# Optimization experiments

Hardware: AMD Instinct MI355X
Metric: run time of the kernel (lower is better)

## Reference

```python
import jax, jax.numpy as jnp
import numpy as np

N, E, DIN, DOUT = 50000, 800000, 64, 64


def setup_inputs() -> dict:
    key = jax.random.key(0)
    k1, k2, k3, k4, k5 = jax.random.split(key, 5)
    x = jax.random.normal(k1, (N, DIN), dtype=jnp.float32)
    edge_index = jax.random.randint(k2, (2, E), 0, N, dtype=jnp.int64)
    edge_attr = jax.random.uniform(k3, (E,), dtype=jnp.float32)
    # PyG GCNConv params: linear weight (no bias in lin) + conv bias
    W = jax.random.normal(k4, (DIN, DOUT), dtype=jnp.float32) / np.sqrt(DIN)
    b = jax.random.normal(k5, (DOUT,), dtype=jnp.float32) * 0.01
    return {
        "x": x,
        "edge_index": edge_index,
        "edge_attr": edge_attr,
        "return_attention_weights": 0,
        "W": W,
        "b": b,
    }


def reference(x, edge_index, edge_attr, return_attention_weights, W, b):
    # GCNConv(add_self_loops=False, normalize=True), edge_weight = ones.
    # edge_attr / return_attention_weights are unused by the original module.
    n = x.shape[0]
    src, dst = edge_index[0], edge_index[1]
    # in-degree on destination nodes (gcn_norm with ones edge weights)
    deg = jax.ops.segment_sum(jnp.ones_like(src, dtype=x.dtype), dst, num_segments=n)
    dis = jnp.where(deg > 0, jax.lax.rsqrt(jnp.maximum(deg, 1)), jnp.zeros_like(deg))
    norm = dis[src] * dis[dst]  # [E]
    h = x @ W  # [N, DOUT] -- transform before aggregation (in < out would flip, equal here)
    msg = h[src] * norm[:, None]  # [E, DOUT]
    out = jax.ops.segment_sum(msg, dst, num_segments=n) + b  # [N, DOUT]
    return out
```

## Files before the change

### kernel.cpp

```cpp
#include <hip/hip_runtime.h>
#include <stdint.h>


#define CAP   64
#define BSH   7
#define NBMAX 512
#define EPB   4096
#define BCAP  2816
#define NGEMM 1024

typedef float vf4 __attribute__((ext_vector_type(4)));

__device__ __forceinline__ int probe_is64(const void* eidx, int n_edges, int n_nodes) {
    int lane = threadIdx.x & 63;
    const long long* p = (const long long*)eidx;
    int cnt = n_edges < 64 ? n_edges : 64;
    long long v = p[lane % cnt];
    bool ok = (v >= 0) && (v < (long long)n_nodes);
    return (__ballot(ok) == ~0ull) ? 1 : 0;
}

__device__ __forceinline__ int load_idx(const void* eidx, long long i, int is64) {
    if (is64) return (int)((const long long*)eidx)[i];
    return ((const int*)eidx)[i];
}

__device__ __forceinline__ unsigned short f2bf(float v) {
    unsigned u = __float_as_uint(v);
    unsigned r = (u + 0x7fffu + ((u >> 16) & 1u)) >> 16;
    return (unsigned short)r;
}

__device__ __forceinline__ float bflo(unsigned u) { return __uint_as_float(u << 16); }
__device__ __forceinline__ float bfhi(unsigned u) { return __uint_as_float(u & 0xffff0000u); }

__global__ __launch_bounds__(256) void k_front(
    const float* __restrict__ x, const float* __restrict__ W,
    unsigned* __restrict__ h32w,
    const void* eidx, unsigned* __restrict__ tails,
    unsigned* __restrict__ buckets,
    int n, int ne, int nb, int nchunks, int binb)
{
    const int tid = (int)threadIdx.x;
    const int bid = (int)blockIdx.x;

    if (bid < binb) {
        __shared__ unsigned histo[NBMAX];
        __shared__ unsigned base[NBMAX];
        int is64 = probe_is64(eidx, ne, n);
        for (int c = bid; c < nchunks; c += binb) {
            __syncthreads();
            for (int i = tid; i < NBMAX; i += 256) histo[i] = 0u;
            __syncthreads();
            unsigned pk[16], rk[16];
            long long e0 = (long long)c * EPB + tid;
            #pragma unroll
            for (int j = 0; j < 16; ++j) {
                long long e = e0 + 256 * j;
                if (e < (long long)ne) {
                    int s = load_idx(eidx, e, is64);
                    int t = load_idx(eidx, (long long)ne + e, is64);
                    pk[j] = ((unsigned)t << 16) | (unsigned)s;
                    rk[j] = atomicAdd(&histo[(unsigned)t >> BSH], 1u);
                } else { pk[j] = 0u; rk[j] = 0xFFFFFFFFu; }
            }
            __syncthreads();
            unsigned U = tails[NBMAX];
            for (int b2 = tid; b2 < nb; b2 += 256) {
                unsigned cc = histo[b2];
                base[b2] = cc ? (atomicAdd(&tails[b2], cc) - U) : 0u;
            }
            __syncthreads();
            #pragma unroll
            for (int j = 0; j < 16; ++j) {
                if (rk[j] != 0xFFFFFFFFu) {
                    unsigned bk = pk[j] >> (16 + BSH);
                    unsigned slot = base[bk] + rk[j];
                    if (slot < (unsigned)BCAP)
                        buckets[(size_t)bk * BCAP + slot] = pk[j];
                }
            }
        }
        return;
    }

    __shared__ float Ws[64][66];
    __shared__ float xs[16][64];
    for (int j = 0; j < 4; ++j) {
        int q = tid + 256 * j;
        int r = q >> 4, c4 = (q & 15) * 4;
        float4 w4 = ((const float4*)W)[q];
        Ws[r][c4] = w4.x; Ws[r][c4 + 1] = w4.y; Ws[r][c4 + 2] = w4.z; Ws[r][c4 + 3] = w4.w;
    }
    const int ntile = (n + 15) >> 4;
    const int f2 = (tid & 31) * 2;
    const int rg = tid >> 5;
    for (int tile = bid - binb; tile < ntile; tile += NGEMM) {
        __syncthreads();
        int row0 = tile << 4;
        {
            int r = tid >> 4, c4 = (tid & 15) * 4;
            int row = row0 + r;
            float4 v4 = (row < n) ? ((const float4*)x)[(size_t)row * 16 + (tid & 15)]
                                  : make_float4(0.f, 0.f, 0.f, 0.f);
            xs[r][c4] = v4.x; xs[r][c4 + 1] = v4.y; xs[r][c4 + 2] = v4.z; xs[r][c4 + 3] = v4.w;
        }
        __syncthreads();
        float a00 = 0.f, a01 = 0.f, a10 = 0.f, a11 = 0.f;
        for (int k = 0; k < 64; ++k) {
            float w0 = Ws[k][f2], w1 = Ws[k][f2 + 1];
            float xa = xs[rg][k], xb = xs[rg + 8][k];
            a00 += xa * w0; a01 += xa * w1;
            a10 += xb * w0; a11 += xb * w1;
        }
        int rowA = row0 + rg, rowB = rowA + 8;
        if (rowA < n)
            h32w[(size_t)rowA * 32 + (f2 >> 1)] =
                (unsigned)f2bf(a00) | ((unsigned)f2bf(a01) << 16);
        if (rowB < n)
            h32w[(size_t)rowB * 32 + (f2 >> 1)] =
                (unsigned)f2bf(a10) | ((unsigned)f2bf(a11) << 16);
    }
}

__global__ __launch_bounds__(256) void k_place2(
    const unsigned* __restrict__ tails,
    const unsigned* __restrict__ buckets,
    unsigned short* __restrict__ csr16,
    float* __restrict__ dis, unsigned char* __restrict__ endc, int n)
{
    __shared__ unsigned degL[1 << BSH];
    const int tid = (int)threadIdx.x;
    const int b = (int)blockIdx.x;
    const int t0 = b << BSH;
    if (tid < (1 << BSH)) degL[tid] = 0u;
    __syncthreads();
    unsigned U = tails[NBMAX];
    unsigned cnt = tails[b] - U;
    if (cnt > (unsigned)BCAP) cnt = (unsigned)BCAP;
    for (unsigned i = (unsigned)tid; i < cnt; i += 256) {
        unsigned p = buckets[(size_t)b * BCAP + i];
        unsigned dl = (p >> 16) & ((1u << BSH) - 1);
        unsigned r = atomicAdd(&degL[dl], 1u);
        if (r < (unsigned)CAP)
            csr16[((size_t)(t0 + (int)dl)) * CAP + r] = (unsigned short)(p & 0xFFFFu);
    }
    __syncthreads();
    if (tid < (1 << BSH)) {
        int node = t0 + tid;
        if (node < n) {
            unsigned d = degL[tid];
            dis[node] = d ? rsqrtf((float)d) : 0.f;
            endc[node] = (unsigned char)(d < (unsigned)CAP ? d : (unsigned)CAP);
        }
    }
}

__global__ __launch_bounds__(256) void k_place_direct(
    const void* eidx, unsigned* __restrict__ deg,
    unsigned short* __restrict__ csr16, int n, int ne)
{
    int is64 = probe_is64(eidx, ne, n);
    unsigned base = deg[n];
    int e = (int)blockIdx.x * 256 + (int)threadIdx.x;
    if (e >= ne) return;
    int s = load_idx(eidx, e, is64);
    int t = load_idx(eidx, (long long)ne + e, is64);
    unsigned r = atomicAdd(&deg[t], 1u) - base;
    if (r < (unsigned)CAP)
        csr16[(size_t)t * CAP + r] = (unsigned short)s;
}

__global__ __launch_bounds__(256) void k_finalize_direct(
    const unsigned* __restrict__ deg,
    float* __restrict__ dis, unsigned char* __restrict__ endc, int n)
{
    int i = (int)blockIdx.x * 256 + (int)threadIdx.x;
    if (i >= n) return;
    unsigned base = deg[n];
    unsigned cnt = deg[i] - base;
    dis[i] = cnt ? rsqrtf((float)cnt) : 0.f;
    endc[i] = (unsigned char)(cnt < (unsigned)CAP ? cnt : (unsigned)CAP);
}

__global__ __launch_bounds__(256) void k_aggregate(
    const float* __restrict__ dis,
    const unsigned char* __restrict__ endc,
    const unsigned short* __restrict__ csr16,
    const uint2* __restrict__ h64,
    const float* __restrict__ bias,
    float* __restrict__ out, int n)
{
    int wid  = (int)threadIdx.x >> 6;
    int lane = (int)threadIdx.x & 63;
    int t = (int)blockIdx.x * 4 + wid;
    if (t >= n) return;
    int allsrc = (int)csr16[(size_t)t * CAP + lane];
    unsigned end = endc[t];
    float dis_t = dis[t];
    int f = lane & 15, q = lane >> 4;
    float a0 = 0.f, a1 = 0.f, a2 = 0.f, a3 = 0.f;

    unsigned K4 = end >> 4;
    for (unsigned k = 0; k < K4; ++k) {
        int j = q + (int)(k << 4);
        int s0 = __shfl(allsrc, j, 64);
        int s1 = __shfl(allsrc, j + 4, 64);
        int s2 = __shfl(allsrc, j + 8, 64);
        int s3 = __shfl(allsrc, j + 12, 64);
        float w0 = dis[s0], w1 = dis[s1], w2 = dis[s2], w3 = dis[s3];
        uint2 u0 = h64[(size_t)s0 * 16 + f];
        uint2 u1 = h64[(size_t)s1 * 16 + f];
        uint2 u2 = h64[(size_t)s2 * 16 + f];
        uint2 u3 = h64[(size_t)s3 * 16 + f];
        a0 += w0 * bflo(u0.x) + w1 * bflo(u1.x) + w2 * bflo(u2.x) + w3 * bflo(u3.x);
        a1 += w0 * bfhi(u0.x) + w1 * bfhi(u1.x) + w2 * bfhi(u2.x) + w3 * bfhi(u3.x);
        a2 += w0 * bflo(u0.y) + w1 * bflo(u1.y) + w2 * bflo(u2.y) + w3 * bflo(u3.y);
        a3 += w0 * bfhi(u0.y) + w1 * bfhi(u1.y) + w2 * bfhi(u2.y) + w3 * bfhi(u3.y);
    }
    unsigned rem = end & 15u;
    if (rem) {
        unsigned jb = K4 << 4;
        for (unsigned k = 0; k < 4; ++k) {
            unsigned jj = jb + (k << 2) + (unsigned)q;
            bool valid = jj < end;
            int s = __shfl(allsrc, (int)(jj & 63u), 64);
            s = valid ? s : 0;
            float w = valid ? dis[s] : 0.f;
            uint2 u = h64[(size_t)s * 16 + f];
            a0 += w * bflo(u.x);
            a1 += w * bfhi(u.x);
            a2 += w * bflo(u.y);
            a3 += w * bfhi(u.y);
        }
    }
    a0 += __shfl_xor(a0, 16, 64); a0 += __shfl_xor(a0, 32, 64);
    a1 += __shfl_xor(a1, 16, 64); a1 += __shfl_xor(a1, 32, 64);
    a2 += __shfl_xor(a2, 16, 64); a2 += __shfl_xor(a2, 32, 64);
    a3 += __shfl_xor(a3, 16, 64); a3 += __shfl_xor(a3, 32, 64);
    if (q == 0) {
        float4 bb = ((const float4*)bias)[f];
        float4 o;
        o.x = a0 * dis_t + bb.x;
        o.y = a1 * dis_t + bb.y;
        o.z = a2 * dis_t + bb.z;
        o.w = a3 * dis_t + bb.w;
        ((float4*)out)[(size_t)t * 16 + f] = o;
    }
}

extern "C" void kernel_launch(void* const* d_in, const int* in_sizes, int n_in,
                              void* d_out, int out_size, void* d_ws, size_t ws_size,
                              hipStream_t stream) {
    const float* x   = (const float*)d_in[0];
    const void* eidx = d_in[1];
    const float* W   = (const float*)d_in[4];
    const float* b   = (const float*)d_in[5];
    float* out       = (float*)d_out;

    const int n  = in_sizes[0] / 64;
    const int ne = in_sizes[2];
    const int nb = (n + (1 << BSH) - 1) >> BSH;
    const int nchunks = (ne + EPB - 1) / EPB;
    const int binb = nchunks;

    auto al = [](size_t v) { return (v + 255) & ~(size_t)255; };

    size_t need = al((size_t)(NBMAX + 1) * 4) + al((size_t)nb * BCAP * 4)
                + al((size_t)n * CAP * 2) + al((size_t)n * 32 * 4)
                + al((size_t)n * 4) + al((size_t)n);
    bool binned = (ws_size >= need) && (nb <= NBMAX);

    char* base = (char*)d_ws;
    size_t off = 0;
    unsigned*       tails   = (unsigned*)(base + off);       off = al(off + (size_t)(NBMAX + 1) * 4);
    unsigned*       buckets = (unsigned*)(base + off);       off = al(off + (size_t)nb * BCAP * 4);
    unsigned short* csr16   = (unsigned short*)(base + off); off = al(off + (size_t)n * CAP * 2);
    unsigned*       h32     = (unsigned*)(base + off);       off = al(off + (size_t)n * 32 * 4);
    float*          dis     = (float*)(base + off);          off = al(off + (size_t)n * 4);
    unsigned char*  endc    = (unsigned char*)(base + off);  off = al(off + (size_t)n);

    if (binned) {
        k_front<<<binb + NGEMM, 256, 0, stream>>>(x, W, h32, eidx, tails, buckets,
                                                  n, ne, nb, nchunks, binb);
        k_place2<<<nb, 256, 0, stream>>>(tails, buckets, csr16, dis, endc, n);
    } else {
        unsigned* deg = buckets;
        k_front<<<0 + NGEMM, 256, 0, stream>>>(x, W, h32, eidx, tails, buckets,
                                               n, ne, nb, 0, 0);
        k_place_direct<<<(ne + 255) / 256, 256, 0, stream>>>(eidx, deg, csr16, n, ne);
        k_finalize_direct<<<(n + 255) / 256, 256, 0, stream>>>(deg, dis, endc, n);
    }
    k_aggregate<<<(n + 3) / 4, 256, 0, stream>>>(dis, endc, csr16, (const uint2*)h32, b, out, n);
}
```

Baseline: 136.0 us.

## Split fused bin+GEMM kernel and use 4x4 register-tiled GEMM

The combined front kernel, which ran edge binning and the x@W transform in different blocks of one launch, is split into two separate kernels. The GEMM now processes 64 rows per block, with each thread computing a 4x4 output tile using vector loads of W from shared memory. This replaces the old 16-row tile with a 2x2 per-thread tile, so each shared-memory load feeds more FMAs. The split removes the overlap that came from co-scheduling binning and GEMM blocks and adds one extra kernel launch.

```diff
diff --git a/kernel.cpp b/kernel.cpp
--- a/kernel.cpp
+++ b/kernel.cpp
@@ -7,7 +7,6 @@
 #define NBMAX 512
 #define EPB   4096
 #define BCAP  2816
-#define NGEMM 1024
 
 typedef float vf4 __attribute__((ext_vector_type(4)));
 
@@ -34,92 +33,102 @@
 __device__ __forceinline__ float bflo(unsigned u) { return __uint_as_float(u << 16); }
 __device__ __forceinline__ float bfhi(unsigned u) { return __uint_as_float(u & 0xffff0000u); }
 
-__global__ __launch_bounds__(256) void k_front(
+__global__ __launch_bounds__(256) void k_bin(
+    const void* eidx, unsigned* __restrict__ tails,
+    unsigned* __restrict__ buckets, int n, int ne, int nb)
+{
+    __shared__ unsigned histo[NBMAX];
+    __shared__ unsigned base[NBMAX];
+    const int tid = (int)threadIdx.x;
+    for (int i = tid; i < NBMAX; i += 256) histo[i] = 0u;
+    int is64 = probe_is64(eidx, ne, n);
+    __syncthreads();
+
+    unsigned pk[16], rk[16];
+    long long e0 = (long long)blockIdx.x * EPB + tid;
+    #pragma unroll
+    for (int j = 0; j < 16; ++j) {
+        long long e = e0 + 256 * j;
+        if (e < (long long)ne) {
+            int s = load_idx(eidx, e, is64);
+            int t = load_idx(eidx, (long long)ne + e, is64);
+            pk[j] = ((unsigned)t << 16) | (unsigned)s;
+            rk[j] = atomicAdd(&histo[(unsigned)t >> BSH], 1u);
+        } else { pk[j] = 0u; rk[j] = 0xFFFFFFFFu; }
+    }
+    __syncthreads();
+    unsigned U = tails[NBMAX];
+    for (int b2 = tid; b2 < nb; b2 += 256) {
+        unsigned cc = histo[b2];
+        base[b2] = cc ? (atomicAdd(&tails[b2], cc) - U) : 0u;
+    }
+    __syncthreads();
+    #pragma unroll
+    for (int j = 0; j < 16; ++j) {
+        if (rk[j] != 0xFFFFFFFFu) {
+            unsigned bk = pk[j] >> (16 + BSH);
+            unsigned slot = base[bk] + rk[j];
+            if (slot < (unsigned)BCAP)
+                buckets[(size_t)bk * BCAP + slot] = pk[j];
+        }
+    }
+}
+
+__global__ __launch_bounds__(256) void k_gemm(
     const float* __restrict__ x, const float* __restrict__ W,
-    unsigned* __restrict__ h32w,
-    const void* eidx, unsigned* __restrict__ tails,
-    unsigned* __restrict__ buckets,
-    int n, int ne, int nb, int nchunks, int binb)
-{
+    unsigned* __restrict__ h32w, int n)
+{
+    __shared__ float Ws[64 * 64];
+    __shared__ float xs[64 * 68];
     const int tid = (int)threadIdx.x;
-    const int bid = (int)blockIdx.x;
-
-    if (bid < binb) {
-        __shared__ unsigned histo[NBMAX];
-        __shared__ unsigned base[NBMAX];
-        int is64 = probe_is64(eidx, ne, n);
-        for (int c = bid; c < nchunks; c += binb) {
-            __syncthreads();
-            for (int i = tid; i < NBMAX; i += 256) histo[i] = 0u;
-            __syncthreads();
-            unsigned pk[16], rk[16];
-            long long e0 = (long long)c * EPB + tid;
-            #pragma unroll
-            for (int j = 0; j < 16; ++j) {
-                long long e = e0 + 256 * j;
-                if (e < (long long)ne) {
-                    int s = load_idx(eidx, e, is64);
-                    int t = load_idx(eidx, (long long)ne + e, is64);
-                    pk[j] = ((unsigned)t << 16) | (unsigned)s;
-                    rk[j] = atomicAdd(&histo[(unsigned)t >> BSH], 1u);
-                } else { pk[j] = 0u; rk[j] = 0xFFFFFFFFu; }
-            }
-            __syncthreads();
-            unsigned U = tails[NBMAX];
-            for (int b2 = tid; b2 < nb; b2 += 256) {
-                unsigned cc = histo[b2];
-                base[b2] = cc ? (atomicAdd(&tails[b2], cc) - U) : 0u;
-            }
-            __syncthreads();
-            #pragma unroll
-            for (int j = 0; j < 16; ++j) {
-                if (rk[j] != 0xFFFFFFFFu) {
-                    unsigned bk = pk[j] >> (16 + BSH);
-                    unsigned slot = base[bk] + rk[j];
-                    if (slot < (unsigned)BCAP)
-                        buckets[(size_t)bk * BCAP + slot] = pk[j];
-                }
-            }
-        }
-        return;
-    }
-
-    __shared__ float Ws[64][66];
-    __shared__ float xs[16][64];
+    const int row0 = (int)blockIdx.x * 64;
+
+    for (int j = 0; j < 4; ++j) {
+        int q = tid + 256 * j;
+        float4 w4 = ((const float4*)W)[q];
+        float* d = &Ws[q * 4];
+        d[0] = w4.x; d[1] = w4.y; d[2] = w4.z; d[3] = w4.w;
+    }
     for (int j = 0; j < 4; ++j) {
         int q = tid + 256 * j;
         int r = q >> 4, c4 = (q & 15) * 4;
-        float4 w4 = ((const float4*)W)[q];
-        Ws[r][c4] = w4.x; Ws[r][c4 + 1] = w4.y; Ws[r][c4 + 2] = w4.z; Ws[r][c4 + 3] = w4.w;
-    }
-    const int ntile = (n + 15) >> 4;
-    const int f2 = (tid & 31) * 2;
-    const int rg = tid >> 5;
-    for (int tile = bid - binb; tile < ntile; tile += NGEMM) {
-        __syncthreads();
-        int row0 = tile << 4;
-        {
-            int r = tid >> 4, c4 = (tid & 15) * 4;
-            int row = row0 + r;
-            float4 v4 = (row < n) ? ((const float4*)x)[(size_t)row * 16 + (tid & 15)]
-                                  : make_float4(0.f, 0.f, 0.f, 0.f);
-            xs[r][c4] = v4.x; xs[r][c4 + 1] = v4.y; xs[r][c4 + 2] = v4.z; xs[r][c4 + 3] = v4.w;
+        int row = row0 + r;
+        float4 v4 = (row < n) ? ((const float4*)x)[(size_t)row * 16 + (q & 15)]
+                              : make_float4(0.f, 0.f, 0.f, 0.f);
+        float* d = &xs[r * 68 + c4];
+        d[0] = v4.x; d[1] = v4.y; d[2] = v4.z; d[3] = v4.w;
+    }
+    __syncthreads();
+
+    const int fg = tid & 15, rg = tid >> 4;
+    const int r0 = rg * 4;
+    float acc[4][4];
+    #pragma unroll
+    for (int i = 0; i < 4; ++i)
+        #pragma unroll
+        for (int j = 0; j < 4; ++j) acc[i][j] = 0.f;
+
+    #pragma unroll 4
+    for (int k = 0; k < 64; ++k) {
+        vf4 w4 = *(const vf4*)&Ws[k * 64 + fg * 4];
+        float x0 = xs[(r0 + 0) * 68 + k];
+        float x1 = xs[(r0 + 1) * 68 + k];
+        float x2 = xs[(r0 + 2) * 68 + k];
+        float x3 = xs[(r0 + 3) * 68 + k];
+        acc[0][0] += x0 * w4.x; acc[0][1] += x0 * w4.y; acc[0][2] += x0 * w4.z; acc[0][3] += x0 * w4.w;
+        acc[1][0] += x1 * w4.x; acc[1][1] += x1 * w4.y; acc[1][2] += x1 * w4.z; acc[1][3] += x1 * w4.w;
+        acc[2][0] += x2 * w4.x; acc[2][1] += x2 * w4.y; acc[2][2] += x2 * w4.z; acc[2][3] += x2 * w4.w;
+        acc[3][0] += x3 * w4.x; acc[3][1] += x3 * w4.y; acc[3][2] += x3 * w4.z; acc[3][3] += x3 * w4.w;
+    }
+    #pragma unroll
+    for (int i = 0; i < 4; ++i) {
+        int row = row0 + r0 + i;
+        if (row < n) {
+            h32w[(size_t)row * 32 + fg * 2] =
+                (unsigned)f2bf(acc[i][0]) | ((unsigned)f2bf(acc[i][1]) << 16);
+            h32w[(size_t)row * 32 + fg * 2 + 1] =
+                (unsigned)f2bf(acc[i][2]) | ((unsigned)f2bf(acc[i][3]) << 16);
         }
-        __syncthreads();
-        float a00 = 0.f, a01 = 0.f, a10 = 0.f, a11 = 0.f;
-        for (int k = 0; k < 64; ++k) {
-            float w0 = Ws[k][f2], w1 = Ws[k][f2 + 1];
-            float xa = xs[rg][k], xb = xs[rg + 8][k];
-            a00 += xa * w0; a01 += xa * w1;
-            a10 += xb * w0; a11 += xb * w1;
-        }
-        int rowA = row0 + rg, rowB = rowA + 8;
-        if (rowA < n)
-            h32w[(size_t)rowA * 32 + (f2 >> 1)] =
-                (unsigned)f2bf(a00) | ((unsigned)f2bf(a01) << 16);
-        if (rowB < n)
-            h32w[(size_t)rowB * 32 + (f2 >> 1)] =
-                (unsigned)f2bf(a10) | ((unsigned)f2bf(a11) << 16);
     }
 }
 
@@ -262,7 +271,6 @@
     const int ne = in_sizes[2];
     const int nb = (n + (1 << BSH) - 1) >> BSH;
     const int nchunks = (ne + EPB - 1) / EPB;
-    const int binb = nchunks;
 
     auto al = [](size_t v) { return (v + 255) & ~(size_t)255; };
 
@@ -281,13 +289,12 @@
     unsigned char*  endc    = (unsigned char*)(base + off);  off = al(off + (size_t)n);
 
     if (binned) {
-        k_front<<<binb + NGEMM, 256, 0, stream>>>(x, W, h32, eidx, tails, buckets,
-                                                  n, ne, nb, nchunks, binb);
+        k_bin<<<nchunks, 256, 0, stream>>>(eidx, tails, buckets, n, ne, nb);
+        k_gemm<<<(n + 63) / 64, 256, 0, stream>>>(x, W, h32, n);
         k_place2<<<nb, 256, 0, stream>>>(tails, buckets, csr16, dis, endc, n);
     } else {
         unsigned* deg = buckets;
-        k_front<<<0 + NGEMM, 256, 0, stream>>>(x, W, h32, eidx, tails, buckets,
-                                               n, ne, nb, 0, 0);
+        k_gemm<<<(n + 63) / 64, 256, 0, stream>>>(x, W, h32, n);
         k_place_direct<<<(ne + 255) / 256, 256, 0, stream>>>(eidx, deg, csr16, n, ne);
         k_finalize_direct<<<(n + 255) / 256, 256, 0, stream>>>(deg, dis, endc, n);
     }
```

After: 125.3 us. 1.09x faster.
